# Performance work log

Hardware: AMD Instinct MI355X
Metric: run time of the kernel (lower is better)

Reference implementation:

```python
import jax, jax.numpy as jnp
import numpy as np

DT = 1e-3
TAU_SYN_INV = 200.0      # 1/5e-3
TAU_MEM_INV = 100.0      # 1/1e-2
TAU_ADAPT_INV = 1.0 / 700.0
V_TH = 1.0
BETA = 1.8
ALPHA = 100.0            # SuperSpike surrogate slope
SEQ_LEN = 40
SCALE = 50.0


@jax.custom_vjp
def superspike(x):
    return (x > 0).astype(x.dtype)

def _ss_fwd(x):
    return (x > 0).astype(x.dtype), x

def _ss_bwd(x, g):
    # SuperSpike surrogate gradient: 1 / (alpha*|x| + 1)^2
    return (g / (ALPHA * jnp.abs(x) + 1.0) ** 2,)

superspike.defvjp(_ss_fwd, _ss_bwd)


def lif_encode(current):
    """Constant-current LIF encoder: current [B,F] -> spikes [T,B,F]."""
    def step(v, _):
        v = v + DT * TAU_MEM_INV * (-v + current)   # v_leak = 0
        z = superspike(v - V_TH)
        v = (1.0 - z) * v                           # reset to v_reset = 0
        return v, z
    _, spikes = jax.lax.scan(step, jnp.zeros_like(current), None, length=SEQ_LEN)
    return spikes


def setup_inputs() -> dict:
    key = jax.random.key(0)
    kx, k1, k2, k3, kd = jax.random.split(key, 5)
    B, S, H, O = 16384, 4, 128, 2
    x = jax.random.normal(kx, (B, S), jnp.float32)
    w_in = jax.random.normal(k1, (H, 2 * S), jnp.float32) * np.sqrt(2.0 / H).astype(np.float32)
    w_rec = jax.random.normal(k2, (H, H), jnp.float32) * np.sqrt(2.0 / H).astype(np.float32)
    w_out = jax.random.normal(k3, (O, H), jnp.float32) * np.sqrt(2.0 / O).astype(np.float32)
    keep = jax.random.bernoulli(kd, 0.5, (SEQ_LEN, B, H))
    drop_mask = keep.astype(jnp.float32) * 2.0      # inverted dropout, p=0.5
    return {"x": x, "w_in": w_in, "w_rec": w_rec, "w_out": w_out,
            "drop_mask": drop_mask}


def reference(x, w_in, w_rec, w_out, drop_mask):
    # Encode state into pos/neg spike trains: [T, B, 2*S]
    x_pos = lif_encode(jax.nn.relu(SCALE * x))
    x_neg = lif_encode(jax.nn.relu(-SCALE * x))
    inp = jnp.concatenate([x_pos, x_neg], axis=2)

    B = x.shape[0]
    H = w_in.shape[0]
    O = w_out.shape[0]
    zH = jnp.zeros((B, H), x.dtype)
    zO = jnp.zeros((B, O), x.dtype)
    carry0 = (zH, zH, zH, zH, zO, zO)  # (z, v, i, b, v_out, i_out)

    def step(carry, xs):
        z, v, i, b, vo, io = carry
        x_t, m_t = xs
        # --- LSNN cell (norse lsnn_step) ---
        v_dec = v + DT * TAU_MEM_INV * (-v + i)        # v_leak = 0
        i_dec = i - DT * TAU_SYN_INV * i
        b_dec = b + DT * TAU_ADAPT_INV * (V_TH - b)
        z_new = superspike(v_dec - b_dec)
        v_new = (1.0 - z_new) * v_dec                  # v_reset = 0
        i_new = i_dec + x_t @ w_in.T + z @ w_rec.T
        b_new = b_dec + z_new * (TAU_ADAPT_INV * BETA)
        # dropout (training mode, p=0.5, precomputed inverted mask)
        z_d = z_new * m_t
        # --- LI readout (norse li_step) ---
        vo_new = vo + DT * TAU_MEM_INV * (-vo + io)
        io_new = io - DT * TAU_SYN_INV * io + z_d @ w_out.T
        return (z_new, v_new, i_new, b_new, vo_new, io_new), vo_new

    _, voltages = jax.lax.scan(step, carry0, (inp, drop_mask))  # [T, B, O]
    m = jnp.max(voltages, axis=0)
    return jax.nn.softmax(m, axis=1)
```

## Files before the change

### kernel.cpp

```cpp
#include <hip/hip_runtime.h>
#include <math.h>
#include <string.h>

#define TSTEPS 40
#define BTOT   16384
#define HDIM   128
#define BT     32
#define ZSTR   168
#define NWAVE  8

typedef __attribute__((ext_vector_type(8))) short bf16x8;
typedef __attribute__((ext_vector_type(4))) float f32x4;

__device__ __forceinline__ short f2bf(float f) {
    unsigned int u; memcpy(&u, &f, 4);
    u += 0x7fffu + ((u >> 16) & 1u);
    return (short)(u >> 16);
}
__device__ __forceinline__ float bf2f(short s) {
    unsigned int u = ((unsigned int)(unsigned short)s) << 16;
    float f; memcpy(&f, &u, 4);
    return f;
}
__device__ __forceinline__ void gload_lds16(const float* g, void* lds) {
    __builtin_amdgcn_global_load_lds(
        (const __attribute__((address_space(1))) void*)g,
        (__attribute__((address_space(3))) void*)lds, 16, 0, 0);
}

__global__ __launch_bounds__(512, 2)
void lsnn6(const float* __restrict__ x,
           const float* __restrict__ w_in,
           const float* __restrict__ w_rec,
           const float* __restrict__ w_out,
           const float* __restrict__ dm,
           float* __restrict__ out)
{
    __shared__ short zbuf[2][BT][ZSTR];
    __shared__ float dmb[2][BT * HDIM];
    __shared__ float red[2][NWAVE][BT][2];

    const int tid   = threadIdx.x;
    const int l     = tid & 63;
    const int wv    = tid >> 6;
    const int li    = l & 15;
    const int q     = l >> 4;
    const int bbase = blockIdx.x * BT;
    const int hcol  = wv * 16 + li;

    bf16x8 wB[5][3];
    #pragma unroll
    for (int kt = 0; kt < 4; ++kt) {
        const float* src = w_rec + hcol * HDIM + kt * 32 + q * 8;
        #pragma unroll
        for (int i = 0; i < 8; ++i) {
            float w0 = src[i];
            short h0 = f2bf(w0); float r1 = w0 - bf2f(h0);
            short h1 = f2bf(r1); float r2 = r1 - bf2f(h1);
            wB[kt][0][i] = h0; wB[kt][1][i] = h1; wB[kt][2][i] = f2bf(r2);
        }
    }
    #pragma unroll
    for (int i = 0; i < 8; ++i) { wB[4][0][i] = 0; wB[4][1][i] = 0; wB[4][2][i] = 0; }
    if (q == 0) {
        const float* src = w_in + hcol * 8;
        #pragma unroll
        for (int i = 0; i < 8; ++i) {
            float w0 = src[i];
            short h0 = f2bf(w0); float r1 = w0 - bf2f(h0);
            short h1 = f2bf(r1); float r2 = r1 - bf2f(h1);
            wB[4][0][i] = h0; wB[4][1][i] = h1; wB[4][2][i] = f2bf(r2);
        }
    }
    const float wo0 = w_out[hcol];
    const float wo1 = w_out[HDIM + hcol];

    f32x4 v[2], cu[2], ba[2];
    #pragma unroll
    for (int rt = 0; rt < 2; ++rt) {
        v[rt]  = (f32x4){0.f,0.f,0.f,0.f};
        cu[rt] = (f32x4){0.f,0.f,0.f,0.f};
        ba[rt] = (f32x4){0.f,0.f,0.f,0.f};
    }

    float ve = 0.f, ce = 0.f;
    if (tid < 256) {
        float xv = 50.f * x[(bbase + (tid >> 3)) * 4 + (tid & 3)];
        ce = ((tid & 7) < 4) ? fmaxf(xv, 0.f) : fmaxf(-xv, 0.f);
    }

    float vo = 0.f, io = 0.f, mx = 0.f;

    const float KA = 1.4285714285714286e-06f;
    const float KB = 2.5714285714285714e-03f;

    for (int idx = tid; idx < 2 * BT * ZSTR; idx += 512) ((short*)zbuf)[idx] = 0;
    for (int idx = tid; idx < NWAVE * BT * 2; idx += 512) ((float*)red)[idx] = 0.f;
    __syncthreads();

    if (tid < 256) {
        float vv = ve + 0.1f * (ce - ve);
        float sp = (vv - 1.0f > 0.f) ? 1.f : 0.f;
        ve = (1.f - sp) * vv;
        zbuf[0][tid >> 3][128 + (tid & 7)] = (sp > 0.5f) ? (short)0x3F80 : (short)0;
    }
    {
        const float* g = dm + (size_t)bbase * HDIM;
        char* lb = (char*)&dmb[0][0];
        gload_lds16(g + tid * 4, lb + tid * 16);
        gload_lds16(g + 2048 + tid * 4, lb + 8192 + tid * 16);
    }

    for (int t = 0; t < TSTEPS; ++t) {
        const int p = t & 1;
        __syncthreads();

        {
            int tn = (t + 1 < TSTEPS) ? t + 1 : TSTEPS - 1;
            const float* g = dm + ((size_t)tn * BTOT + bbase) * HDIM;
            char* lb = (char*)&dmb[1 - p][0];
            gload_lds16(g + tid * 4, lb + tid * 16);
            gload_lds16(g + 2048 + tid * 4, lb + 8192 + tid * 16);
        }

        if (wv == 0) {
            int row = l >> 1, o = l & 1;
            float s = 0.f;
            #pragma unroll
            for (int w = 0; w < NWAVE; ++w) s += red[p][w][row][o];
            float von = vo + 0.1f * (io - vo);
            io = io - 0.2f * io + s;
            vo = von;
            mx = fmaxf(mx, vo);
        }

        if (tid < 256) {
            float vv = ve + 0.1f * (ce - ve);
            float sp = (vv - 1.0f > 0.f) ? 1.f : 0.f;
            ve = (1.f - sp) * vv;
            zbuf[1 - p][tid >> 3][128 + (tid & 7)] = (sp > 0.5f) ? (short)0x3F80 : (short)0;
        }

        f32x4 acc[2];
        #pragma unroll
        for (int rt = 0; rt < 2; ++rt) {
            f32x4 a = {0.f, 0.f, 0.f, 0.f};
            #pragma unroll
            for (int kt = 0; kt < 5; ++kt) {
                bf16x8 zA = *reinterpret_cast<const bf16x8*>(&zbuf[p][rt * 16 + li][kt * 32 + q * 8]);
                #pragma unroll
                for (int pp = 0; pp < 3; ++pp)
                    a = __builtin_amdgcn_mfma_f32_16x16x32_bf16(zA, wB[kt][pp], a, 0, 0, 0);
            }
            acc[rt] = a;
        }

        #pragma unroll
        for (int rt = 0; rt < 2; ++rt) {
            float p0r[4], p1r[4];
            #pragma unroll
            for (int r = 0; r < 4; ++r) {
                int row = rt * 16 + q * 4 + r;
                float vd = v[rt][r] + 0.1f * (cu[rt][r] - v[rt][r]);
                float id = cu[rt][r] - 0.2f * cu[rt][r];
                float bd = ba[rt][r] + KA * (1.0f - ba[rt][r]);
                float z  = (vd - bd > 0.f) ? 1.f : 0.f;
                v[rt][r]  = (1.f - z) * vd;
                ba[rt][r] = bd + z * KB;
                cu[rt][r] = id + acc[rt][r];
                zbuf[1 - p][row][hcol] = (z > 0.5f) ? (short)0x3F80 : (short)0;
                float zd = z * dmb[p][row * HDIM + hcol];
                p0r[r] = zd * wo0;
                p1r[r] = zd * wo1;
            }
            #pragma unroll
            for (int s = 1; s < 16; s <<= 1) {
                #pragma unroll
                for (int r = 0; r < 4; ++r) {
                    p0r[r] += __shfl_xor(p0r[r], s);
                    p1r[r] += __shfl_xor(p1r[r], s);
                }
            }
            if (li == 0) {
                #pragma unroll
                for (int r = 0; r < 4; ++r) {
                    red[1 - p][wv][rt * 16 + q * 4 + r][0] = p0r[r];
                    red[1 - p][wv][rt * 16 + q * 4 + r][1] = p1r[r];
                }
            }
        }
    }

    __syncthreads();
    if (wv == 0) {
        int row = l >> 1, o = l & 1;
        float s = 0.f;
        #pragma unroll
        for (int w = 0; w < NWAVE; ++w) s += red[TSTEPS & 1][w][row][o];
        float von = vo + 0.1f * (io - vo);
        vo = von;
        mx = fmaxf(mx, vo);
        float other = __shfl_xor(mx, 1);
        float mmax  = fmaxf(mx, other);
        float e  = expf(mx - mmax);
        float eo = expf(other - mmax);
        out[(size_t)(bbase + row) * 2 + o] = e / (e + eo);
    }
}

extern "C" void kernel_launch(void* const* d_in, const int* in_sizes, int n_in,
                              void* d_out, int out_size, void* d_ws, size_t ws_size,
                              hipStream_t stream) {
    const float* x     = (const float*)d_in[0];
    const float* w_in  = (const float*)d_in[1];
    const float* w_rec = (const float*)d_in[2];
    const float* w_out = (const float*)d_in[3];
    const float* dmask = (const float*)d_in[4];
    float* outp = (float*)d_out;

    lsnn6<<<BTOT / BT, 512, 0, stream>>>(x, w_in, w_rec, w_out, dmask, outp);
}
```

Before: 560.1 us.

## Defer readout to post-loop MFMA over ballot-packed dropout spike bitmasks

Removes the per-step readout reduction (shuffle tree plus cross-wave LDS sums) from the recurrent loop. Each step now records a ballot bitmask of spikes that survive dropout, keeping the mask as a 0/2 threshold. After the loop, MFMA with a two-part bf16 split of w_out forms the readout inputs for all timesteps, and one wave runs the scalar LI recurrence and max. Dropout masks are now loaded straight into registers with strided global loads instead of async global-to-LDS copies. This shortens the serial loop body but relies on the mask being exactly 0 or 2, and the bf16 split of w_out reduces precision slightly.

Result: faster. 460.2 us (-17.8%).

```diff
diff --git a/kernel.cpp b/kernel.cpp
--- a/kernel.cpp
+++ b/kernel.cpp
@@ -11,6 +11,7 @@
 
 typedef __attribute__((ext_vector_type(8))) short bf16x8;
 typedef __attribute__((ext_vector_type(4))) float f32x4;
+typedef __attribute__((ext_vector_type(4))) unsigned int u32x4;
 
 __device__ __forceinline__ short f2bf(float f) {
     unsigned int u; memcpy(&u, &f, 4);
@@ -22,14 +23,9 @@
     float f; memcpy(&f, &u, 4);
     return f;
 }
-__device__ __forceinline__ void gload_lds16(const float* g, void* lds) {
-    __builtin_amdgcn_global_load_lds(
-        (const __attribute__((address_space(1))) void*)g,
-        (__attribute__((address_space(3))) void*)lds, 16, 0, 0);
-}
 
 __global__ __launch_bounds__(512, 2)
-void lsnn6(const float* __restrict__ x,
+void lsnn7(const float* __restrict__ x,
            const float* __restrict__ w_in,
            const float* __restrict__ w_rec,
            const float* __restrict__ w_out,
@@ -37,8 +33,8 @@
            float* __restrict__ out)
 {
     __shared__ short zbuf[2][BT][ZSTR];
-    __shared__ float dmb[2][BT * HDIM];
-    __shared__ float red[2][NWAVE][BT][2];
+    __shared__ unsigned short maskb[TSTEPS][BT][NWAVE];
+    __shared__ float sbuf[TSTEPS][BT][2];
 
     const int tid   = threadIdx.x;
     const int l     = tid & 63;
@@ -72,8 +68,6 @@
             wB[4][0][i] = h0; wB[4][1][i] = h1; wB[4][2][i] = f2bf(r2);
         }
     }
-    const float wo0 = w_out[hcol];
-    const float wo1 = w_out[HDIM + hcol];
 
     f32x4 v[2], cu[2], ba[2];
     #pragma unroll
@@ -89,13 +83,10 @@
         ce = ((tid & 7) < 4) ? fmaxf(xv, 0.f) : fmaxf(-xv, 0.f);
     }
 
-    float vo = 0.f, io = 0.f, mx = 0.f;
-
     const float KA = 1.4285714285714286e-06f;
     const float KB = 2.5714285714285714e-03f;
 
     for (int idx = tid; idx < 2 * BT * ZSTR; idx += 512) ((short*)zbuf)[idx] = 0;
-    for (int idx = tid; idx < NWAVE * BT * 2; idx += 512) ((float*)red)[idx] = 0.f;
     __syncthreads();
 
     if (tid < 256) {
@@ -104,34 +95,29 @@
         ve = (1.f - sp) * vv;
         zbuf[0][tid >> 3][128 + (tid & 7)] = (sp > 0.5f) ? (short)0x3F80 : (short)0;
     }
+    float mr[2][4];
     {
-        const float* g = dm + (size_t)bbase * HDIM;
-        char* lb = (char*)&dmb[0][0];
-        gload_lds16(g + tid * 4, lb + tid * 16);
-        gload_lds16(g + 2048 + tid * 4, lb + 8192 + tid * 16);
+        const float* dmt = dm + (size_t)bbase * HDIM;
+        #pragma unroll
+        for (int rt = 0; rt < 2; ++rt)
+            #pragma unroll
+            for (int r = 0; r < 4; ++r)
+                mr[rt][r] = dmt[(rt * 16 + q * 4 + r) * HDIM + hcol];
     }
 
     for (int t = 0; t < TSTEPS; ++t) {
         const int p = t & 1;
         __syncthreads();
 
+        float mrn[2][4];
         {
             int tn = (t + 1 < TSTEPS) ? t + 1 : TSTEPS - 1;
-            const float* g = dm + ((size_t)tn * BTOT + bbase) * HDIM;
-            char* lb = (char*)&dmb[1 - p][0];
-            gload_lds16(g + tid * 4, lb + tid * 16);
-            gload_lds16(g + 2048 + tid * 4, lb + 8192 + tid * 16);
-        }
-
-        if (wv == 0) {
-            int row = l >> 1, o = l & 1;
-            float s = 0.f;
-            #pragma unroll
-            for (int w = 0; w < NWAVE; ++w) s += red[p][w][row][o];
-            float von = vo + 0.1f * (io - vo);
-            io = io - 0.2f * io + s;
-            vo = von;
-            mx = fmaxf(mx, vo);
+            const float* dmn = dm + ((size_t)tn * BTOT + bbase) * HDIM;
+            #pragma unroll
+            for (int rt = 0; rt < 2; ++rt)
+                #pragma unroll
+                for (int r = 0; r < 4; ++r)
+                    mrn[rt][r] = dmn[(rt * 16 + q * 4 + r) * HDIM + hcol];
         }
 
         if (tid < 256) {
@@ -157,10 +143,9 @@
 
         #pragma unroll
         for (int rt = 0; rt < 2; ++rt) {
-            float p0r[4], p1r[4];
             #pragma unroll
             for (int r = 0; r < 4; ++r) {
-                int row = rt * 16 + q * 4 + r;
+                const int row = rt * 16 + q * 4 + r;
                 float vd = v[rt][r] + 0.1f * (cu[rt][r] - v[rt][r]);
                 float id = cu[rt][r] - 0.2f * cu[rt][r];
                 float bd = ba[rt][r] + KA * (1.0f - ba[rt][r]);
@@ -169,37 +154,67 @@
                 ba[rt][r] = bd + z * KB;
                 cu[rt][r] = id + acc[rt][r];
                 zbuf[1 - p][row][hcol] = (z > 0.5f) ? (short)0x3F80 : (short)0;
-                float zd = z * dmb[p][row * HDIM + hcol];
-                p0r[r] = zd * wo0;
-                p1r[r] = zd * wo1;
+                unsigned long long bm = __ballot((z > 0.5f) && (mr[rt][r] > 1.0f));
+                if (li == 0)
+                    maskb[t][row][wv] = (unsigned short)(bm >> (q * 16));
             }
-            #pragma unroll
-            for (int s = 1; s < 16; s <<= 1) {
-                #pragma unroll
-                for (int r = 0; r < 4; ++r) {
-                    p0r[r] += __shfl_xor(p0r[r], s);
-                    p1r[r] += __shfl_xor(p1r[r], s);
-                }
-            }
-            if (li == 0) {
-                #pragma unroll
-                for (int r = 0; r < 4; ++r) {
-                    red[1 - p][wv][rt * 16 + q * 4 + r][0] = p0r[r];
-                    red[1 - p][wv][rt * 16 + q * 4 + r][1] = p1r[r];
-                }
-            }
-        }
+        }
+        #pragma unroll
+        for (int rt = 0; rt < 2; ++rt)
+            #pragma unroll
+            for (int r = 0; r < 4; ++r) mr[rt][r] = mrn[rt][r];
     }
 
     __syncthreads();
+    asm volatile("" ::: "memory");
+
+    bf16x8 woB[4][2];
+    #pragma unroll
+    for (int kt = 0; kt < 4; ++kt) {
+        #pragma unroll
+        for (int i = 0; i < 8; ++i) {
+            float w0 = 0.f;
+            if (li < 2) w0 = w_out[li * HDIM + kt * 32 + q * 8 + i];
+            short h0 = f2bf(w0);
+            woB[kt][0][i] = h0;
+            woB[kt][1][i] = f2bf(w0 - bf2f(h0));
+        }
+    }
+    for (int T = wv; T < TSTEPS * 2; T += NWAVE) {
+        const int t  = T >> 1;
+        const int rt = T & 1;
+        f32x4 ac = {0.f, 0.f, 0.f, 0.f};
+        #pragma unroll
+        for (int kt = 0; kt < 4; ++kt) {
+            unsigned b = (unsigned)maskb[t][rt * 16 + li][2 * kt + (q >> 1)];
+            b = (b >> ((q & 1) * 8)) & 0xffu;
+            u32x4 aw;
+            aw.x = ((b & 1u)   << 14) | ((b & 2u)   << 29);
+            aw.y = ((b & 4u)   << 12) | ((b & 8u)   << 27);
+            aw.z = ((b & 16u)  << 10) | ((b & 32u)  << 25);
+            aw.w = ((b & 64u)  <<  8) | ((b & 128u) << 23);
+            bf16x8 A = __builtin_bit_cast(bf16x8, aw);
+            ac = __builtin_amdgcn_mfma_f32_16x16x32_bf16(A, woB[kt][0], ac, 0, 0, 0);
+            ac = __builtin_amdgcn_mfma_f32_16x16x32_bf16(A, woB[kt][1], ac, 0, 0, 0);
+        }
+        if (li < 2) {
+            #pragma unroll
+            for (int r = 0; r < 4; ++r)
+                sbuf[t][rt * 16 + q * 4 + r][li] = ac[r];
+        }
+    }
+    __syncthreads();
+
     if (wv == 0) {
-        int row = l >> 1, o = l & 1;
-        float s = 0.f;
-        #pragma unroll
-        for (int w = 0; w < NWAVE; ++w) s += red[TSTEPS & 1][w][row][o];
-        float von = vo + 0.1f * (io - vo);
-        vo = von;
-        mx = fmaxf(mx, vo);
+        const int row = l >> 1, o = l & 1;
+        float vo = 0.f, io = 0.f, mx = 0.f;
+        for (int t = 0; t < TSTEPS; ++t) {
+            float s = sbuf[t][row][o];
+            float von = vo + 0.1f * (io - vo);
+            io = io - 0.2f * io + s;
+            vo = von;
+            mx = fmaxf(mx, vo);
+        }
         float other = __shfl_xor(mx, 1);
         float mmax  = fmaxf(mx, other);
         float e  = expf(mx - mmax);
@@ -218,5 +233,5 @@
     const float* dmask = (const float*)d_in[4];
     float* outp = (float*)d_out;
 
-    lsnn6<<<BTOT / BT, 512, 0, stream>>>(x, w_in, w_rec, w_out, dmask, outp);
-}
+    lsnn7<<<BTOT / BT, 512, 0, stream>>>(x, w_in, w_rec, w_out, dmask, outp);
+}
```
